# Optimization experiments

Measured on AMD Instinct MI355X. Metric: run time of the kernel, lower is better.

Reference implementation:

```python
import math
import jax, jax.numpy as jnp
import numpy as np

FACTOR = 1

def setup_inputs() -> dict:
    key = jax.random.key(0)
    k1, k2, k3 = jax.random.split(key, 3)
    B, N, L, H, E = 4, 207, 96, 8, 64
    queries = jax.random.normal(k1, (B, N, L, H, E), dtype=jnp.float32)
    keys = jax.random.normal(k2, (B, N, L, H, E), dtype=jnp.float32)
    values = jax.random.normal(k3, (B, N, L, H, E), dtype=jnp.float32)
    return {"queries": queries, "keys": keys, "values": values, "attn_mask": 0}


def _autocorr(queries, keys, values):
    B, N, L, H, E = queries.shape
    # L == S here, so no padding/truncation branch is needed.
    q = jnp.transpose(queries, (0, 1, 3, 4, 2))  # [B,N,H,E,L]
    k = jnp.transpose(keys, (0, 1, 3, 4, 2))
    v = jnp.transpose(values, (0, 1, 3, 4, 2))   # [B,N,H,D,L]
    qf = jnp.fft.rfft(q, axis=-1)
    kf = jnp.fft.rfft(k, axis=-1)
    corr = jnp.fft.irfft(qf * jnp.conj(kf), n=L, axis=-1)  # [B,N,H,E,L]
    top_k = int(FACTOR * math.log(L))  # = 4 for L=96
    weights, delay = jax.lax.top_k(corr, top_k)            # [B,N,H,E,k]
    tmp_corr = jax.nn.softmax(weights, axis=-1)
    init_index = jnp.arange(L)[None, None, None, None, :]
    agg = jnp.zeros_like(v)
    for i in range(top_k):  # small fixed k, circular shift via modular gather
        idx = (init_index + delay[..., i:i+1]) % L
        pattern = jnp.take_along_axis(v, idx, axis=-1)
        agg = agg + pattern * tmp_corr[..., i:i+1]
    V = jnp.transpose(agg, (0, 1, 4, 2, 3))      # [B,N,L,H,D]
    return V, jnp.transpose(corr, (0, 1, 4, 2, 3))


def reference(queries, keys, values, attn_mask):
    return _autocorr(queries, keys, values)
```

## Files before the change

### kernel.cpp

```cpp
#include <hip/hip_runtime.h>


namespace {
constexpr int Lx = 96;
constexpr int Hx = 8;
constexpr int Ex = 64;
constexpr int HE = Hx * Ex;
constexpr int NBH = 4 * 207 * Hx;
constexpr long OUT1 = 4L * 207 * Lx * Hx * Ex;
constexpr int KP = 66;
constexpr int VP = 66;
}

__device__ __forceinline__ void sel_max(float av, int ai, float bv, int bi,
                                        float& ov, int& oi) {
  bool ta = (av > bv) || ((av == bv) && (ai < bi));
  ov = ta ? av : bv;
  oi = ta ? ai : bi;
}

__device__ __forceinline__ void cswap_desc(float& xv, int& xi, float& yv, int& yi) {
  bool sw = (yv > xv) || ((yv == xv) && (yi < xi));
  float nxv = sw ? yv : xv, nyv = sw ? xv : yv;
  int nxi = sw ? yi : xi, nyi = sw ? xi : yi;
  xv = nxv; yv = nyv; xi = nxi; yi = nyi;
}

__global__ __launch_bounds__(256, 3) void autocorr_kernel(
    const float* __restrict__ qg,
    const float* __restrict__ kg,
    const float* __restrict__ vg,
    float* __restrict__ outV,
    float* __restrict__ outC) {
  __shared__ __align__(16) float sK[Lx * KP];
  __shared__ __align__(16) float sV[Lx * VP];

  const int tid = threadIdx.x;
  const int bid = blockIdx.x;
  const int bn = bid >> 3;
  const int h = bid & 7;
  const int base = bn * (Lx * HE) + h * Ex;

#pragma unroll
  for (int i = 0; i < 6; ++i) {
    int f = i * 256 + tid;
    int t = f >> 4;
    int e4 = (f & 15) << 2;
    int g = base + t * HE + e4;
    float4 kv = *reinterpret_cast<const float4*>(kg + g);
    float4 vv = *reinterpret_cast<const float4*>(vg + g);
    int s = t * KP + e4;
    *reinterpret_cast<float2*>(sK + s)     = make_float2(kv.x, kv.y);
    *reinterpret_cast<float2*>(sK + s + 2) = make_float2(kv.z, kv.w);
    *reinterpret_cast<float2*>(sV + s)     = make_float2(vv.x, vv.y);
    *reinterpret_cast<float2*>(sV + s + 2) = make_float2(vv.z, vv.w);
  }
  __syncthreads();

  const int e = tid >> 2;
  const int tb = tid & 3;
  const int tau0 = tb * 24;

  float acc[24];
#pragma unroll
  for (int j = 0; j < 24; ++j) acc[j] = 0.0f;

  const float* qp = qg + base + e;
  const float* kcol = sK + e;

  float kvp[24];
  {
    int r0 = ((-1 - tb) & 3) * 24;
#pragma unroll
    for (int m = 0; m < 24; ++m) kvp[m] = kcol[(r0 + m) * KP];
  }

#pragma unroll 1
  for (int c = 0; c < 4; ++c) {
    int r0 = ((c - tb) & 3) * 24;
    float kv[24], qv[24];
#pragma unroll
    for (int tt = 0; tt < 24; ++tt) {
      kv[tt] = kcol[(r0 + tt) * KP];
      qv[tt] = qp[(c * 24 + tt) * HE];
    }
#pragma unroll
    for (int tt = 0; tt < 24; ++tt) {
      float qt = qv[tt];
#pragma unroll
      for (int j = 0; j <= tt; ++j) acc[j] += qt * kv[tt - j];
#pragma unroll
      for (int j = tt + 1; j < 24; ++j) acc[j] += qt * kvp[tt - j + 24];
    }
#pragma unroll
    for (int m = 0; m < 24; ++m) kvp[m] = kv[m];
  }

  float v0 = -__builtin_inff(), v1 = v0, v2 = v0, v3 = v0;
  int i0 = 0, i1 = 0, i2 = 0, i3 = 0;
#pragma unroll
  for (int j = 0; j < 24; ++j) {
    float nv = acc[j];
    int ni = tau0 + j;
    if (nv > v0) { v3 = v2; i3 = i2; v2 = v1; i2 = i1; v1 = v0; i1 = i0; v0 = nv; i0 = ni; }
    else if (nv > v1) { v3 = v2; i3 = i2; v2 = v1; i2 = i1; v1 = nv; i1 = ni; }
    else if (nv > v2) { v3 = v2; i3 = i2; v2 = nv; i2 = ni; }
    else if (nv > v3) { v3 = nv; i3 = ni; }
  }

#pragma unroll
  for (int m = 1; m <= 2; m <<= 1) {
    float b0 = __shfl_xor(v0, m, 64);
    float b1 = __shfl_xor(v1, m, 64);
    float b2 = __shfl_xor(v2, m, 64);
    float b3 = __shfl_xor(v3, m, 64);
    int j0 = __shfl_xor(i0, m, 64);
    int j1 = __shfl_xor(i1, m, 64);
    int j2 = __shfl_xor(i2, m, 64);
    int j3 = __shfl_xor(i3, m, 64);
    float t0, t1, t2, t3;
    int u0, u1, u2, u3;
    sel_max(v0, i0, b3, j3, t0, u0);
    sel_max(v1, i1, b2, j2, t1, u1);
    sel_max(v2, i2, b1, j1, t2, u2);
    sel_max(v3, i3, b0, j0, t3, u3);
    cswap_desc(t0, u0, t2, u2);
    cswap_desc(t1, u1, t3, u3);
    cswap_desc(t0, u0, t1, u1);
    cswap_desc(t2, u2, t3, u3);
    v0 = t0; v1 = t1; v2 = t2; v3 = t3;
    i0 = u0; i1 = u1; i2 = u2; i3 = u3;
  }

  float w1 = __expf(v1 - v0);
  float w2 = __expf(v2 - v0);
  float w3 = __expf(v3 - v0);
  float inv = 1.0f / (1.0f + w1 + w2 + w3);
  float w0 = inv;
  w1 *= inv; w2 *= inv; w3 *= inv;

#pragma unroll
  for (int j = 0; j < 24; ++j) {
    int t = tau0 + j;
    int g = base + t * HE + e;
    outC[g] = acc[j];
    int t0 = t + i0; if (t0 >= 96) t0 -= 96;
    int t1 = t + i1; if (t1 >= 96) t1 -= 96;
    int t2 = t + i2; if (t2 >= 96) t2 -= 96;
    int t3 = t + i3; if (t3 >= 96) t3 -= 96;
    float r = w0 * sV[t0 * VP + e];
    r += w1 * sV[t1 * VP + e];
    r += w2 * sV[t2 * VP + e];
    r += w3 * sV[t3 * VP + e];
    outV[g] = r;
  }
}

extern "C" void kernel_launch(void* const* d_in, const int* in_sizes, int n_in,
                              void* d_out, int out_size, void* d_ws, size_t ws_size,
                              hipStream_t stream) {
  const float* q = (const float*)d_in[0];
  const float* k = (const float*)d_in[1];
  const float* v = (const float*)d_in[2];
  float* out = (float*)d_out;
  autocorr_kernel<<<dim3(NBH), dim3(256), 0, stream>>>(q, k, v, out, out + OUT1);
}
```

Baseline: 675.3 us.

## Remap threads so each wavefront covers all 64 channels, merge top-k via LDS

Thread mapping changes so lane index is the channel and wavefront index is the lag block. Each wavefront's query loads and its correlation and output stores become contiguous 64-float rows. Because the four lag blocks of one channel now sit in different wavefronts, the top-4 merge moves from shuffles to a shared-memory candidate exchange. That adds an extra barrier and a redundant LDS copy. Shared arrays drop their padding, the K double-buffer is unrolled into two alternating register sets, and the V gather uses hoisted base pointers.

```diff
diff --git a/kernel.cpp b/kernel.cpp
--- a/kernel.cpp
+++ b/kernel.cpp
@@ -8,22 +8,6 @@
 constexpr int HE = Hx * Ex;
 constexpr int NBH = 4 * 207 * Hx;
 constexpr long OUT1 = 4L * 207 * Lx * Hx * Ex;
-constexpr int KP = 66;
-constexpr int VP = 66;
-}
-
-__device__ __forceinline__ void sel_max(float av, int ai, float bv, int bi,
-                                        float& ov, int& oi) {
-  bool ta = (av > bv) || ((av == bv) && (ai < bi));
-  ov = ta ? av : bv;
-  oi = ta ? ai : bi;
-}
-
-__device__ __forceinline__ void cswap_desc(float& xv, int& xi, float& yv, int& yi) {
-  bool sw = (yv > xv) || ((yv == xv) && (yi < xi));
-  float nxv = sw ? yv : xv, nyv = sw ? xv : yv;
-  int nxi = sw ? yi : xi, nyi = sw ? xi : yi;
-  xv = nxv; yv = nyv; xi = nxi; yi = nyi;
 }
 
 __global__ __launch_bounds__(256, 3) void autocorr_kernel(
@@ -32,8 +16,9 @@
     const float* __restrict__ vg,
     float* __restrict__ outV,
     float* __restrict__ outC) {
-  __shared__ __align__(16) float sK[Lx * KP];
-  __shared__ __align__(16) float sV[Lx * VP];
+  __shared__ __align__(16) float S[12288];
+  float* sV = S;
+  float* sK = S + 6144;
 
   const int tid = threadIdx.x;
   const int bid = blockIdx.x;
@@ -49,51 +34,62 @@
     int g = base + t * HE + e4;
     float4 kv = *reinterpret_cast<const float4*>(kg + g);
     float4 vv = *reinterpret_cast<const float4*>(vg + g);
-    int s = t * KP + e4;
-    *reinterpret_cast<float2*>(sK + s)     = make_float2(kv.x, kv.y);
-    *reinterpret_cast<float2*>(sK + s + 2) = make_float2(kv.z, kv.w);
-    *reinterpret_cast<float2*>(sV + s)     = make_float2(vv.x, vv.y);
-    *reinterpret_cast<float2*>(sV + s + 2) = make_float2(vv.z, vv.w);
+    *reinterpret_cast<float4*>(sK + t * 64 + e4) = kv;
+    *reinterpret_cast<float4*>(sV + t * 64 + e4) = vv;
   }
   __syncthreads();
 
-  const int e = tid >> 2;
-  const int tb = tid & 3;
+  const int e = tid & 63;
+  const int tb = tid >> 6;
   const int tau0 = tb * 24;
 
   float acc[24];
 #pragma unroll
   for (int j = 0; j < 24; ++j) acc[j] = 0.0f;
 
-  const float* qp = qg + base + e;
   const float* kcol = sK + e;
+  const float* qb = qg + base + e;
 
-  float kvp[24];
-  {
-    int r0 = ((-1 - tb) & 3) * 24;
+  float kp[24], ku[24];
 #pragma unroll
-    for (int m = 0; m < 24; ++m) kvp[m] = kcol[(r0 + m) * KP];
-  }
+  for (int m = 0; m < 24; ++m) kp[m] = kcol[(72 + m) * 64];
 
 #pragma unroll 1
-  for (int c = 0; c < 4; ++c) {
-    int r0 = ((c - tb) & 3) * 24;
-    float kv[24], qv[24];
+  for (int cc = 0; cc < 2; ++cc) {
+    {
+      const int c = 2 * cc;
+      const float* qp = qb + (24 * ((c + tb) & 3)) * HE;
+      float qv[24];
 #pragma unroll
-    for (int tt = 0; tt < 24; ++tt) {
-      kv[tt] = kcol[(r0 + tt) * KP];
-      qv[tt] = qp[(c * 24 + tt) * HE];
+      for (int tt = 0; tt < 24; ++tt) qv[tt] = qp[tt * HE];
+#pragma unroll
+      for (int tt = 0; tt < 24; ++tt) ku[tt] = kcol[(24 * c + tt) * 64];
+#pragma unroll
+      for (int tt = 0; tt < 24; ++tt) {
+        float qt = qv[tt];
+#pragma unroll
+        for (int j = 0; j <= tt; ++j) acc[j] += qt * ku[tt - j];
+#pragma unroll
+        for (int j = tt + 1; j < 24; ++j) acc[j] += qt * kp[24 + tt - j];
+      }
     }
+    {
+      const int c = 2 * cc + 1;
+      const float* qp = qb + (24 * ((c + tb) & 3)) * HE;
+      float qv[24];
 #pragma unroll
-    for (int tt = 0; tt < 24; ++tt) {
-      float qt = qv[tt];
+      for (int tt = 0; tt < 24; ++tt) qv[tt] = qp[tt * HE];
 #pragma unroll
-      for (int j = 0; j <= tt; ++j) acc[j] += qt * kv[tt - j];
+      for (int tt = 0; tt < 24; ++tt) kp[tt] = kcol[(24 * c + tt) * 64];
 #pragma unroll
-      for (int j = tt + 1; j < 24; ++j) acc[j] += qt * kvp[tt - j + 24];
+      for (int tt = 0; tt < 24; ++tt) {
+        float qt = qv[tt];
+#pragma unroll
+        for (int j = 0; j <= tt; ++j) acc[j] += qt * kp[tt - j];
+#pragma unroll
+        for (int j = tt + 1; j < 24; ++j) acc[j] += qt * ku[24 + tt - j];
+      }
     }
-#pragma unroll
-    for (int m = 0; m < 24; ++m) kvp[m] = kv[m];
   }
 
   float v0 = -__builtin_inff(), v1 = v0, v2 = v0, v3 = v0;
@@ -108,28 +104,42 @@
     else if (nv > v3) { v3 = nv; i3 = ni; }
   }
 
+  {
+    float* outCp = outC + base + tau0 * HE + e;
 #pragma unroll
-  for (int m = 1; m <= 2; m <<= 1) {
-    float b0 = __shfl_xor(v0, m, 64);
-    float b1 = __shfl_xor(v1, m, 64);
-    float b2 = __shfl_xor(v2, m, 64);
-    float b3 = __shfl_xor(v3, m, 64);
-    int j0 = __shfl_xor(i0, m, 64);
-    int j1 = __shfl_xor(i1, m, 64);
-    int j2 = __shfl_xor(i2, m, 64);
-    int j3 = __shfl_xor(i3, m, 64);
-    float t0, t1, t2, t3;
-    int u0, u1, u2, u3;
-    sel_max(v0, i0, b3, j3, t0, u0);
-    sel_max(v1, i1, b2, j2, t1, u1);
-    sel_max(v2, i2, b1, j1, t2, u2);
-    sel_max(v3, i3, b0, j0, t3, u3);
-    cswap_desc(t0, u0, t2, u2);
-    cswap_desc(t1, u1, t3, u3);
-    cswap_desc(t0, u0, t1, u1);
-    cswap_desc(t2, u2, t3, u3);
-    v0 = t0; v1 = t1; v2 = t2; v3 = t3;
-    i0 = u0; i1 = u1; i2 = u2; i3 = u3;
+    for (int j = 0; j < 24; ++j) outCp[j * HE] = acc[j];
+  }
+
+  __syncthreads();
+
+  float2* mrg = reinterpret_cast<float2*>(S + 8192);
+  mrg[(tb * 4 + 0) * 64 + e] = make_float2(v0, __int_as_float(i0));
+  mrg[(tb * 4 + 1) * 64 + e] = make_float2(v1, __int_as_float(i1));
+  mrg[(tb * 4 + 2) * 64 + e] = make_float2(v2, __int_as_float(i2));
+  mrg[(tb * 4 + 3) * 64 + e] = make_float2(v3, __int_as_float(i3));
+
+  {
+    float4 a = *reinterpret_cast<const float4*>(S + tid * 4);
+    *reinterpret_cast<float4*>(S + 6144 + tid * 4) = a;
+    int i1c = tid + 256;
+    if (i1c < 368) {
+      float4 b = *reinterpret_cast<const float4*>(S + i1c * 4);
+      *reinterpret_cast<float4*>(S + 6144 + i1c * 4) = b;
+    }
+  }
+  __syncthreads();
+
+  v0 = -__builtin_inff(); v1 = v0; v2 = v0; v3 = v0;
+  i0 = 0; i1 = 0; i2 = 0; i3 = 0;
+#pragma unroll
+  for (int cand = 0; cand < 16; ++cand) {
+    float2 c = mrg[cand * 64 + e];
+    float nv = c.x;
+    int ni = __float_as_int(c.y);
+    if (nv > v0) { v3 = v2; i3 = i2; v2 = v1; i2 = i1; v1 = v0; i1 = i0; v0 = nv; i0 = ni; }
+    else if (nv > v1) { v3 = v2; i3 = i2; v2 = v1; i2 = i1; v1 = nv; i1 = ni; }
+    else if (nv > v2) { v3 = v2; i3 = i2; v2 = nv; i2 = ni; }
+    else if (nv > v3) { v3 = nv; i3 = ni; }
   }
 
   float w1 = __expf(v1 - v0);
@@ -139,20 +149,24 @@
   float w0 = inv;
   w1 *= inv; w2 *= inv; w3 *= inv;
 
+  {
+    int a0 = tau0 + i0; if (a0 >= 96) a0 -= 96;
+    int a1 = tau0 + i1; if (a1 >= 96) a1 -= 96;
+    int a2 = tau0 + i2; if (a2 >= 96) a2 -= 96;
+    int a3 = tau0 + i3; if (a3 >= 96) a3 -= 96;
+    const float* p0 = sV + a0 * 64 + e;
+    const float* p1 = sV + a1 * 64 + e;
+    const float* p2 = sV + a2 * 64 + e;
+    const float* p3 = sV + a3 * 64 + e;
+    float* outVp = outV + base + tau0 * HE + e;
 #pragma unroll
-  for (int j = 0; j < 24; ++j) {
-    int t = tau0 + j;
-    int g = base + t * HE + e;
-    outC[g] = acc[j];
-    int t0 = t + i0; if (t0 >= 96) t0 -= 96;
-    int t1 = t + i1; if (t1 >= 96) t1 -= 96;
-    int t2 = t + i2; if (t2 >= 96) t2 -= 96;
-    int t3 = t + i3; if (t3 >= 96) t3 -= 96;
-    float r = w0 * sV[t0 * VP + e];
-    r += w1 * sV[t1 * VP + e];
-    r += w2 * sV[t2 * VP + e];
-    r += w3 * sV[t3 * VP + e];
-    outV[g] = r;
+    for (int j = 0; j < 24; ++j) {
+      float r = w0 * p0[j * 64];
+      r += w1 * p1[j * 64];
+      r += w2 * p2[j * 64];
+      r += w3 * p3[j * 64];
+      outVp[j * HE] = r;
+    }
   }
 }
 
```

Measured after the change: 676.9 us. About the same (+0.2%).
